# Kernel optimization log

Hardware: AMD Instinct MI355X
Metric: run time of the kernel (lower is better)

Reference implementation:

```python
import jax, jax.numpy as jnp
import numpy as np
from jax import lax

D_MODEL, D_INNER, N_STATE, DT_RANK, K = 1024, 2048, 16, 64, 3
B_SZ, SEQ = 2, 1024

def silu(v):
    return v * jax.nn.sigmoid(v)

def setup_inputs() -> dict:
    key = jax.random.key(0)
    ks = jax.random.split(key, 12)
    s = 0.02
    return {
        'x': jax.random.normal(ks[0], (B_SZ, SEQ, D_MODEL), jnp.float32),
        'A_log': jax.random.normal(ks[1], (D_INNER, N_STATE), jnp.float32) * 0.5,
        'W_in': jax.random.normal(ks[2], (D_MODEL, 2 * D_INNER), jnp.float32) * s,
        'b_in': jax.random.normal(ks[3], (2 * D_INNER,), jnp.float32) * s,
        'conv_w': jax.random.normal(ks[4], (D_INNER, 1, K), jnp.float32) * s,  # depthwise [O,I/g,K]
        'conv_b': jax.random.normal(ks[5], (D_INNER,), jnp.float32) * s,
        'W_x': jax.random.normal(ks[6], (D_INNER, DT_RANK + 2 * N_STATE), jnp.float32) * s,
        'W_dt': jax.random.normal(ks[7], (DT_RANK, D_INNER), jnp.float32) * s,
        'b_dt': jax.random.normal(ks[8], (D_INNER,), jnp.float32) * s,
        'W_out': jax.random.normal(ks[9], (D_INNER, D_MODEL), jnp.float32) * s,
        'b_out': jax.random.normal(ks[10], (D_MODEL,), jnp.float32) * s,
    }

def selective_scan(u, delta, A, B, C):
    # u, delta: [b,l,d]; A: [d,n]; B, C: [b,l,n]
    deltaA = jnp.exp(jnp.einsum('bld,dn->bldn', delta, A))          # [b,l,d,n]
    deltaBu = jnp.einsum('bld,bln,bld->bldn', delta, B, u)           # [b,l,d,n]
    h0 = jnp.zeros((u.shape[0], u.shape[2], A.shape[1]), u.dtype)    # [b,d,n]
    def step(h, inp):
        dA_t, dBu_t, C_t = inp
        h = dA_t * h + dBu_t
        y = jnp.einsum('bdn,bn->bd', h, C_t)
        return h, y
    xs = (jnp.moveaxis(deltaA, 1, 0), jnp.moveaxis(deltaBu, 1, 0), jnp.moveaxis(C, 1, 0))
    _, ys = lax.scan(step, h0, xs)                                   # [l,b,d]
    return jnp.moveaxis(ys, 0, 1)                                    # [b,l,d]

def reference(x, A_log, W_in, b_in, conv_w, conv_b, W_x, W_dt, b_dt, W_out, b_out):
    xr = x @ W_in + b_in                                             # [b,l,2*d_inner]
    u, res = jnp.split(xr, 2, axis=-1)
    # causal depthwise conv1d (pad left k-1, truncate == torch pad=k-1 then slice)
    uc = lax.conv_general_dilated(
        jnp.moveaxis(u, 1, 2), conv_w, window_strides=(1,),
        padding=[(K - 1, 0)], feature_group_count=D_INNER,
        dimension_numbers=('NCH', 'OIH', 'NCH'))
    u = silu(jnp.moveaxis(uc, 2, 1) + conv_b)                        # [b,l,d_inner]
    xp = u @ W_x                                                     # [b,l,dt_rank+2n]
    dt, Bm, Cm = jnp.split(xp, [DT_RANK, DT_RANK + N_STATE], axis=-1)
    delta = jax.nn.softplus(dt @ W_dt + b_dt)                        # [b,l,d_inner]
    A = -jnp.exp(A_log)                                              # [d_inner,n]
    y = selective_scan(u, delta, A, Bm, Cm)                          # [b,l,d_inner]
    y = y * silu(res)
    return y @ W_out + b_out
```

## Files before the change

### kernel.cpp

```cpp
#include <hip/hip_runtime.h>

#define D_MODEL 1024
#define D_INNER 2048
#define N_ST    16
#define DT_RANK 64
#define BSZ     2
#define SEQL    1024
#define NTOK    (BSZ*SEQL)
#define NC      64
#define LC      (SEQL/NC)

typedef __attribute__((ext_vector_type(4))) float f32x4;
typedef __attribute__((ext_vector_type(8))) short bf16x8;

__device__ __forceinline__ short f2b(float f) {
  unsigned u = __builtin_bit_cast(unsigned, f);
  u += 0x7fffu + ((u >> 16) & 1u);
  return (short)(u >> 16);
}

__device__ __forceinline__ float b2f(unsigned short s) {
  return __builtin_bit_cast(float, (unsigned)s << 16);
}

__device__ __forceinline__ void gload16(const void* g, void* l) {
  __builtin_amdgcn_global_load_lds(
      (const __attribute__((address_space(1))) void*)g,
      (__attribute__((address_space(3))) void*)l, 16, 0, 0);
}

template<int SOFTPLUS, int PARTIAL, int RESSPLIT, int OUTB16>
__global__ __launch_bounds__(256)
void gemm_kernel(const short* __restrict__ A, const short* __restrict__ Bm,
                 const float* __restrict__ bias, float* __restrict__ C,
                 short* __restrict__ upb, short* __restrict__ resb,
                 int M, int N, int K, int lda, int ldb, int ldc, int kChunk)
{
  __shared__ short sA[2][128 * 64];
  __shared__ short sB[2][128 * 64];
  const int tid  = threadIdx.x;
  const int lane = tid & 63;
  const int wave = tid >> 6;
  const int wr = wave >> 1, wc = wave & 1;
  const int lr = lane & 15, lg = lane >> 4;
  const int m0 = blockIdx.y * 128;
  const int n0 = blockIdx.x * 128;
  const int kStart = blockIdx.z * kChunk;
  int kEnd = kStart + kChunk; if (kEnd > K) kEnd = K;
  const int nt = (kEnd - kStart) >> 6;

  if (PARTIAL) C += (size_t)blockIdx.z * M * ldc;

  const int srow = lane >> 3;
  const int scol = ((lane & 7) ^ srow) * 8;
  const short* aS = A + (size_t)(m0 + wave * 32 + srow) * lda + scol + kStart;
  const short* bS = Bm + (size_t)(n0 + wave * 32 + srow) * ldb + scol + kStart;
  const int ldsOff = wave * 2048;

#define STAGE(buf, koff)                                                   \
  {                                                                        \
    _Pragma("unroll")                                                      \
    for (int i_ = 0; i_ < 4; ++i_) {                                       \
      gload16(aS + (size_t)(i_ * 8) * lda + (koff), &sA[buf][ldsOff + i_ * 512]); \
      gload16(bS + (size_t)(i_ * 8) * ldb + (koff), &sB[buf][ldsOff + i_ * 512]); \
    }                                                                      \
  }

  f32x4 acc[4][4];
#pragma unroll
  for (int i = 0; i < 4; ++i)
#pragma unroll
    for (int j = 0; j < 4; ++j) acc[i][j] = (f32x4){0.f, 0.f, 0.f, 0.f};

  STAGE(0, 0);

  for (int t = 0; t < nt; ++t) {
    const int cur = t & 1;
    if (t + 1 < nt) {
      STAGE(cur ^ 1, (t + 1) * 64);
      asm volatile("s_waitcnt vmcnt(8)" ::: "memory");
    } else {
      asm volatile("s_waitcnt vmcnt(0)" ::: "memory");
    }
    __builtin_amdgcn_s_barrier();

#pragma unroll
    for (int kk = 0; kk < 2; ++kk) {
      bf16x8 aF[4], bF[4];
#pragma unroll
      for (int mi = 0; mi < 4; ++mi) {
        const int row = wr * 64 + mi * 16 + lr;
        aF[mi] = *reinterpret_cast<const bf16x8*>(
            &sA[cur][row * 64 + (((kk * 4 + lg) ^ (lr & 7)) * 8)]);
      }
#pragma unroll
      for (int ni = 0; ni < 4; ++ni) {
        const int row = wc * 64 + ni * 16 + lr;
        bF[ni] = *reinterpret_cast<const bf16x8*>(
            &sB[cur][row * 64 + (((kk * 4 + lg) ^ (lr & 7)) * 8)]);
      }
#pragma unroll
      for (int mi = 0; mi < 4; ++mi)
#pragma unroll
        for (int ni = 0; ni < 4; ++ni)
          acc[mi][ni] = __builtin_amdgcn_mfma_f32_16x16x32_bf16(
              aF[mi], bF[ni], acc[mi][ni], 0, 0, 0);
    }
    __builtin_amdgcn_s_barrier();
  }
#undef STAGE

#pragma unroll
  for (int mi = 0; mi < 4; ++mi) {
    const int row = m0 + wr * 64 + mi * 16 + lg * 4;
#pragma unroll
    for (int ni = 0; ni < 4; ++ni) {
      const int col = n0 + wc * 64 + ni * 16 + lr;
      if (RESSPLIT) {
        const float bv = bias[col];
        if (col < 2048) {
#pragma unroll
          for (int j = 0; j < 4; ++j)
            upb[(size_t)(row + j) * 2048 + col] = f2b(acc[mi][ni][j] + bv);
        } else {
#pragma unroll
          for (int j = 0; j < 4; ++j) {
            float v = acc[mi][ni][j] + bv;
            resb[(size_t)(row + j) * 2048 + (col - 2048)] =
                f2b(v / (1.f + __expf(-v)));
          }
        }
      } else if (OUTB16) {
        const float bv = bias[col];
#pragma unroll
        for (int j = 0; j < 4; ++j) {
          float v = acc[mi][ni][j] + bv;
          if (SOFTPLUS) v = fmaxf(v, 0.f) + log1pf(__expf(-fabsf(v)));
          upb[(size_t)(row + j) * ldc + col] = f2b(v);
        }
      } else if (col < N) {
        float bv = (bias != nullptr && blockIdx.z == 0) ? bias[col] : 0.f;
#pragma unroll
        for (int j = 0; j < 4; ++j) {
          float v = acc[mi][ni][j] + bv;
          if (SOFTPLUS) v = fmaxf(v, 0.f) + log1pf(__expf(-fabsf(v)));
          C[(size_t)(row + j) * ldc + col] = v;
        }
      }
    }
  }
}

__device__ __forceinline__ void trans_body(const float* __restrict__ in,
                                           short* __restrict__ out,
                                           int R, int C, int bx, int by,
                                           short (*t)[33], int tidx)
{
  const int c0 = bx * 32, r0 = by * 32;
  const int cc = tidx & 31, rr = tidx >> 5;
#pragma unroll
  for (int i = 0; i < 4; ++i)
    t[rr + i * 8][cc] = f2b(in[(size_t)(r0 + rr + i * 8) * C + c0 + cc]);
  __syncthreads();
#pragma unroll
  for (int i = 0; i < 4; ++i)
    out[(size_t)(c0 + rr + i * 8) * R + r0 + cc] = t[cc][rr + i * 8];
}

#define PB_CAST  2048
#define PB_WIN   4096
#define PB_WX    192
#define PB_WDT   128
#define PB_WOUT  2048

__global__ __launch_bounds__(256)
void prep_kernel(const float* __restrict__ x,    const float* __restrict__ W_in,
                 const float* __restrict__ W_x,  const float* __restrict__ W_dt,
                 const float* __restrict__ W_out,
                 short* __restrict__ xb,  short* __restrict__ Wib,
                 short* __restrict__ Wxb, short* __restrict__ Wdtb,
                 short* __restrict__ Wob)
{
  __shared__ short t[32][33];
  const int bid = blockIdx.x, tidx = threadIdx.x;
  if (bid < PB_CAST) {
    const int i = bid * 256 + tidx;
    float4 v = *reinterpret_cast<const float4*>(x + (size_t)i * 4);
    *reinterpret_cast<short4*>(xb + (size_t)i * 4) =
        make_short4(f2b(v.x), f2b(v.y), f2b(v.z), f2b(v.w));
  } else if (bid < PB_CAST + PB_WIN) {
    const int b = bid - PB_CAST;
    trans_body(W_in, Wib, 1024, 4096, b % 128, b / 128, t, tidx);
  } else if (bid < PB_CAST + PB_WIN + PB_WX) {
    const int b = bid - PB_CAST - PB_WIN;
    trans_body(W_x, Wxb, 2048, 96, b % 3, b / 3, t, tidx);
  } else if (bid < PB_CAST + PB_WIN + PB_WX + PB_WDT) {
    const int b = bid - PB_CAST - PB_WIN - PB_WX;
    trans_body(W_dt, Wdtb, 64, 2048, b % 64, b / 64, t, tidx);
  } else {
    const int b = bid - PB_CAST - PB_WIN - PB_WX - PB_WDT;
    trans_body(W_out, Wob, 2048, 1024, b % 32, b / 32, t, tidx);
  }
}

__global__ __launch_bounds__(256)
void combine16_kernel(const float* __restrict__ part, float* __restrict__ xp,
                      short* __restrict__ dtb)
{
  const int gid = blockIdx.x * 256 + threadIdx.x;
  const int r = gid / 24, q = gid - r * 24;
  float4 s = make_float4(0.f, 0.f, 0.f, 0.f);
#pragma unroll
  for (int c = 0; c < 16; ++c) {
    const float4 v = *reinterpret_cast<const float4*>(
        part + (size_t)c * 2048 * 96 + (size_t)r * 96 + q * 4);
    s.x += v.x; s.y += v.y; s.z += v.z; s.w += v.w;
  }
  *reinterpret_cast<float4*>(xp + (size_t)r * 96 + q * 4) = s;
  if (q < 16)
    *reinterpret_cast<short4*>(dtb + (size_t)r * 64 + q * 4) =
        make_short4(f2b(s.x), f2b(s.y), f2b(s.z), f2b(s.w));
}

__global__ __launch_bounds__(256)
void combine4_kernel(const float* __restrict__ part, const float* __restrict__ bias,
                     float* __restrict__ out)
{
  const int gid = blockIdx.x * 256 + threadIdx.x;
  const int r = gid >> 8, c4 = gid & 255;
  const float4 bv = *reinterpret_cast<const float4*>(bias + c4 * 4);
  float4 s = bv;
#pragma unroll
  for (int z = 0; z < 4; ++z) {
    const float4 v = *reinterpret_cast<const float4*>(
        part + (size_t)z * 2048 * 1024 + (size_t)r * 1024 + c4 * 4);
    s.x += v.x; s.y += v.y; s.z += v.z; s.w += v.w;
  }
  *reinterpret_cast<float4*>(out + (size_t)r * 1024 + c4 * 4) = s;
}

__global__ __launch_bounds__(256)
void conv_silu_kernel(const unsigned short* __restrict__ up, const float* __restrict__ cw,
                      const float* __restrict__ cb, short* __restrict__ ub)
{
  int i  = blockIdx.x * 256 + threadIdx.x;
  int t  = i >> 9;
  int dq = (i & 511) << 2;
  int l  = t & (SEQL - 1);
  float4 w0 = *reinterpret_cast<const float4*>(cw + dq * 3);
  float4 w1 = *reinterpret_cast<const float4*>(cw + dq * 3 + 4);
  float4 w2 = *reinterpret_cast<const float4*>(cw + dq * 3 + 8);
  float4 bb = *reinterpret_cast<const float4*>(cb + dq);
  ushort4 X2 = *reinterpret_cast<const ushort4*>(up + (size_t)t * 2048 + dq);
  ushort4 z4; z4.x = z4.y = z4.z = z4.w = 0;
  ushort4 X1 = (l >= 1) ? *reinterpret_cast<const ushort4*>(up + (size_t)(t - 1) * 2048 + dq) : z4;
  ushort4 X0 = (l >= 2) ? *reinterpret_cast<const ushort4*>(up + (size_t)(t - 2) * 2048 + dq) : z4;
  float r0 = bb.x + w0.x * b2f(X0.x) + w0.y * b2f(X1.x) + w0.z * b2f(X2.x);
  float r1 = bb.y + w0.w * b2f(X0.y) + w1.x * b2f(X1.y) + w1.y * b2f(X2.y);
  float r2 = bb.z + w1.z * b2f(X0.z) + w1.w * b2f(X1.z) + w2.x * b2f(X2.z);
  float r3 = bb.w + w2.y * b2f(X0.w) + w2.z * b2f(X1.w) + w2.w * b2f(X2.w);
  float o0 = r0 / (1.f + __expf(-r0));
  float o1 = r1 / (1.f + __expf(-r1));
  float o2 = r2 / (1.f + __expf(-r2));
  float o3 = r3 / (1.f + __expf(-r3));
  *reinterpret_cast<short4*>(ub + (size_t)t * 2048 + dq) =
      make_short4(f2b(o0), f2b(o1), f2b(o2), f2b(o3));
}

__global__ __launch_bounds__(256, 4)
void scan_pass1(const unsigned short* __restrict__ deltab, const unsigned short* __restrict__ ub,
                const float* __restrict__ xp, const float* __restrict__ A_log,
                float* __restrict__ sdl, float* __restrict__ HS)
{
  const int d = blockIdx.y * 256 + threadIdx.x;
  const int c = blockIdx.x, b = blockIdx.z;
  const int t0 = (b << 10) + c * LC;
  float Ac[16];
#pragma unroll
  for (int q = 0; q < 4; ++q) {
    float4 a = *reinterpret_cast<const float4*>(A_log + (size_t)d * 16 + q * 4);
    Ac[q * 4 + 0] = -__expf(a.x); Ac[q * 4 + 1] = -__expf(a.y);
    Ac[q * 4 + 2] = -__expf(a.z); Ac[q * 4 + 3] = -__expf(a.w);
  }
  float h[16];
#pragma unroll
  for (int n = 0; n < 16; ++n) h[n] = 0.f;
  float sd = 0.f;
  const unsigned short* dp = deltab + (size_t)t0 * 2048 + d;
  const unsigned short* up = ub + (size_t)t0 * 2048 + d;
  const float* xb = xp + (size_t)t0 * 96 + DT_RANK;
#pragma unroll 4
  for (int t = 0; t < LC; ++t) {
    float dl = b2f(dp[(size_t)t * 2048]);
    float ul = b2f(up[(size_t)t * 2048]);
    float Bf[16];
#pragma unroll
    for (int q = 0; q < 4; ++q)
      *reinterpret_cast<float4*>(&Bf[q * 4]) =
          *reinterpret_cast<const float4*>(xb + (size_t)t * 96 + q * 4);
    float dlu = dl * ul;
    sd += dl;
#pragma unroll
    for (int n = 0; n < 16; ++n)
      h[n] = __expf(dl * Ac[n]) * h[n] + dlu * Bf[n];
  }
  sdl[((size_t)b * NC + c) * 2048 + d] = sd;
  float* hs = HS + (((size_t)b * NC + c) * 2048 + d) * 16;
#pragma unroll
  for (int q = 0; q < 4; ++q)
    *reinterpret_cast<float4*>(hs + q * 4) =
        make_float4(h[q * 4], h[q * 4 + 1], h[q * 4 + 2], h[q * 4 + 3]);
}

__global__ __launch_bounds__(256)
void scan_pass2(const float* __restrict__ sdl, const float* __restrict__ A_log,
                float* __restrict__ HS)
{
  const int gid = blockIdx.x * 256 + threadIdx.x;
  const int b = gid >> 15, rest = gid & 32767;
  const int d = rest >> 4;
  const float Ac = -__expf(A_log[rest]);
  float P[NC], S[NC];
#pragma unroll
  for (int c = 0; c < NC; ++c)
    P[c] = sdl[(((size_t)b * NC + c) << 11) + d];
#pragma unroll
  for (int c = 0; c < NC; ++c)
    S[c] = HS[(((size_t)b * NC + c) << 15) + rest];
#pragma unroll
  for (int c = 0; c < NC; ++c)
    P[c] = __expf(P[c] * Ac);
  float h = 0.f;
#pragma unroll
  for (int c = 0; c < NC; ++c) {
    HS[(((size_t)b * NC + c) << 15) + rest] = h;
    h = P[c] * h + S[c];
  }
}

__global__ __launch_bounds__(256, 4)
void scan_pass3(const unsigned short* __restrict__ deltab, const unsigned short* __restrict__ ub,
                const float* __restrict__ xp, const float* __restrict__ A_log,
                const float* __restrict__ HS, const unsigned short* __restrict__ rb,
                short* __restrict__ zb)
{
  const int d = blockIdx.y * 256 + threadIdx.x;
  const int c = blockIdx.x, b = blockIdx.z;
  const int t0 = (b << 10) + c * LC;
  float Ac[16];
#pragma unroll
  for (int q = 0; q < 4; ++q) {
    float4 a = *reinterpret_cast<const float4*>(A_log + (size_t)d * 16 + q * 4);
    Ac[q * 4 + 0] = -__expf(a.x); Ac[q * 4 + 1] = -__expf(a.y);
    Ac[q * 4 + 2] = -__expf(a.z); Ac[q * 4 + 3] = -__expf(a.w);
  }
  float h[16];
  const float* hs = HS + (((size_t)b * NC + c) * 2048 + d) * 16;
#pragma unroll
  for (int q = 0; q < 4; ++q) {
    float4 v = *reinterpret_cast<const float4*>(hs + q * 4);
    h[q * 4 + 0] = v.x; h[q * 4 + 1] = v.y; h[q * 4 + 2] = v.z; h[q * 4 + 3] = v.w;
  }
  const unsigned short* dp = deltab + (size_t)t0 * 2048 + d;
  const unsigned short* up = ub + (size_t)t0 * 2048 + d;
  const float* xb = xp + (size_t)t0 * 96 + DT_RANK;
  const float* xc = xp + (size_t)t0 * 96 + DT_RANK + N_ST;
  const unsigned short* rp = rb + (size_t)t0 * 2048 + d;
  short* zp = zb + (size_t)t0 * 2048 + d;
#pragma unroll 4
  for (int t = 0; t < LC; ++t) {
    float dl = b2f(dp[(size_t)t * 2048]);
    float ul = b2f(up[(size_t)t * 2048]);
    float rv = b2f(rp[(size_t)t * 2048]);
    float Bf[16], Cf[16];
#pragma unroll
    for (int q = 0; q < 4; ++q) {
      *reinterpret_cast<float4*>(&Bf[q * 4]) =
          *reinterpret_cast<const float4*>(xb + (size_t)t * 96 + q * 4);
      *reinterpret_cast<float4*>(&Cf[q * 4]) =
          *reinterpret_cast<const float4*>(xc + (size_t)t * 96 + q * 4);
    }
    float dlu = dl * ul;
    float p0 = 0.f, p1 = 0.f, p2 = 0.f, p3 = 0.f;
#pragma unroll
    for (int n = 0; n < 16; ++n) {
      h[n] = __expf(dl * Ac[n]) * h[n] + dlu * Bf[n];
      float t2 = h[n] * Cf[n];
      if ((n & 3) == 0) p0 += t2;
      else if ((n & 3) == 1) p1 += t2;
      else if ((n & 3) == 2) p2 += t2;
      else p3 += t2;
    }
    float p = (p0 + p1) + (p2 + p3);
    zp[(size_t)t * 2048] = f2b(p * rv);
  }
}

extern "C" void kernel_launch(void* const* d_in, const int* in_sizes, int n_in,
                              void* d_out, int out_size, void* d_ws, size_t ws_size,
                              hipStream_t stream)
{
  const float* x      = (const float*)d_in[0];
  const float* A_log  = (const float*)d_in[1];
  const float* W_in   = (const float*)d_in[2];
  const float* b_in   = (const float*)d_in[3];
  const float* conv_w = (const float*)d_in[4];
  const float* conv_b = (const float*)d_in[5];
  const float* W_x    = (const float*)d_in[6];
  const float* W_dt   = (const float*)d_in[7];
  const float* b_dt   = (const float*)d_in[8];
  const float* W_out  = (const float*)d_in[9];
  const float* b_out  = (const float*)d_in[10];
  float* out = (float*)d_out;

  char* p = (char*)d_ws;
  short* upb    = (short*)p; p += (size_t)NTOK * 2048 * 2;
  short* rb     = (short*)p; p += (size_t)NTOK * 2048 * 2;
  short* ub     = (short*)p; p += (size_t)NTOK * 2048 * 2;
  float* xp     = (float*)p; p += (size_t)NTOK * 96 * 4;
  short* dtb    = (short*)p; p += (size_t)NTOK * 64 * 2;
  short* deltab = (short*)p; p += (size_t)NTOK * 2048 * 2;
  short* zb     = (short*)p; p += (size_t)NTOK * 2048 * 2;
  short* xb     = (short*)p; p += (size_t)NTOK * 1024 * 2;
  short* Wib    = (short*)p; p += (size_t)4096 * 1024 * 2;
  short* Wxb    = (short*)p; p += (size_t)128 * 2048 * 2;
  short* Wdtb   = (short*)p; p += (size_t)2048 * 64 * 2;
  short* Wob    = (short*)p; p += (size_t)1024 * 2048 * 2;
  float* scr    = (float*)p; p += (size_t)4 * 2048 * 1024 * 4;
  float* xppart = scr;
  float* opart  = scr;
  float* sdl    = (float*)p; p += (size_t)BSZ * NC * 2048 * 4;
  float* HS     = (float*)p; p += (size_t)BSZ * NC * 2048 * 16 * 4;

  prep_kernel<<<dim3(PB_CAST + PB_WIN + PB_WX + PB_WDT + PB_WOUT), 256, 0, stream>>>(
      x, W_in, W_x, W_dt, W_out, xb, Wib, Wxb, Wdtb, Wob);

  gemm_kernel<0, 0, 1, 0><<<dim3(32, 16, 1), 256, 0, stream>>>(
      xb, Wib, b_in, nullptr, upb, rb, NTOK, 4096, 1024, 1024, 1024, 0, 1024);
  conv_silu_kernel<<<dim3(4096), 256, 0, stream>>>(
      (const unsigned short*)upb, conv_w, conv_b, ub);
  gemm_kernel<0, 1, 0, 0><<<dim3(1, 16, 16), 256, 0, stream>>>(
      ub, Wxb, nullptr, xppart, nullptr, nullptr, NTOK, 96, 2048, 2048, 2048, 96, 128);
  combine16_kernel<<<dim3(192), 256, 0, stream>>>(xppart, xp, dtb);
  gemm_kernel<1, 0, 0, 1><<<dim3(16, 16, 1), 256, 0, stream>>>(
      dtb, Wdtb, b_dt, nullptr, deltab, nullptr, NTOK, 2048, 64, 64, 64, 2048, 64);
  scan_pass1<<<dim3(NC, 8, BSZ), 256, 0, stream>>>(
      (const unsigned short*)deltab, (const unsigned short*)ub, xp, A_log, sdl, HS);
  scan_pass2<<<dim3(256), 256, 0, stream>>>(sdl, A_log, HS);
  scan_pass3<<<dim3(NC, 8, BSZ), 256, 0, stream>>>(
      (const unsigned short*)deltab, (const unsigned short*)ub, xp, A_log, HS,
      (const unsigned short*)rb, zb);
  gemm_kernel<0, 1, 0, 0><<<dim3(8, 16, 4), 256, 0, stream>>>(
      zb, Wob, nullptr, opart, nullptr, nullptr, NTOK, 1024, 2048, 2048, 2048, 1024, 512);
  combine4_kernel<<<dim3(2048), 256, 0, stream>>>(opart, b_out, out);
}
```

Baseline: 151.3 us.

## Fuse conv+SiLU into in-proj GEMM epilogue, bf16 out partials, fewer scan chunks

The in-projection GEMM now stages its bias-added u tile in LDS and computes the causal depthwise conv and SiLU in its epilogue. A small fixup kernel recomputes the two boundary rows of each 128-row tile. Block indices for that GEMM are remapped for locality. Output-projection split-K partials are stored as bf16 rather than fp32, and the scan chunk count drops from 64 to 32. Together these remove the standalone conv pass and halve partial-sum traffic, at the cost of extra rounding in the partial sums and less scan parallelism.

```diff
diff --git a/kernel.cpp b/kernel.cpp
--- a/kernel.cpp
+++ b/kernel.cpp
@@ -7,7 +7,7 @@
 #define BSZ     2
 #define SEQL    1024
 #define NTOK    (BSZ*SEQL)
-#define NC      64
+#define NC      32
 #define LC      (SEQL/NC)
 
 typedef __attribute__((ext_vector_type(4))) float f32x4;
@@ -34,6 +34,8 @@
 void gemm_kernel(const short* __restrict__ A, const short* __restrict__ Bm,
                  const float* __restrict__ bias, float* __restrict__ C,
                  short* __restrict__ upb, short* __restrict__ resb,
+                 const float* __restrict__ cw, const float* __restrict__ cb,
+                 short* __restrict__ ubuf,
                  int M, int N, int K, int lda, int ldb, int ldc, int kChunk)
 {
   __shared__ short sA[2][128 * 64];
@@ -43,13 +45,18 @@
   const int wave = tid >> 6;
   const int wr = wave >> 1, wc = wave & 1;
   const int lr = lane & 15, lg = lane >> 4;
-  const int m0 = blockIdx.y * 128;
-  const int n0 = blockIdx.x * 128;
+
+  int bx = blockIdx.x, by = blockIdx.y;
+  if (RESSPLIT) {
+    const int lin = by * 32 + bx;
+    const int lb = (lin & 7) * 64 + (lin >> 3);
+    bx = lb >> 4; by = lb & 15;
+  }
+  const int m0 = by * 128;
+  const int n0 = bx * 128;
   const int kStart = blockIdx.z * kChunk;
   int kEnd = kStart + kChunk; if (kEnd > K) kEnd = K;
   const int nt = (kEnd - kStart) >> 6;
-
-  if (PARTIAL) C += (size_t)blockIdx.z * M * ldc;
 
   const int srow = lane >> 3;
   const int scol = ((lane & 7) ^ srow) * 8;
@@ -110,19 +117,54 @@
   }
 #undef STAGE
 
-#pragma unroll
-  for (int mi = 0; mi < 4; ++mi) {
-    const int row = m0 + wr * 64 + mi * 16 + lg * 4;
-#pragma unroll
-    for (int ni = 0; ni < 4; ++ni) {
-      const int col = n0 + wc * 64 + ni * 16 + lr;
-      if (RESSPLIT) {
-        const float bv = bias[col];
-        if (col < 2048) {
-#pragma unroll
-          for (int j = 0; j < 4; ++j)
-            upb[(size_t)(row + j) * 2048 + col] = f2b(acc[mi][ni][j] + bv);
-        } else {
+  if (RESSPLIT) {
+    if (n0 < 2048) {
+      short (*sU)[128] = reinterpret_cast<short (*)[128]>(&sA[0][0]);
+#pragma unroll
+      for (int mi = 0; mi < 4; ++mi) {
+#pragma unroll
+        for (int ni = 0; ni < 4; ++ni) {
+          const int cl = wc * 64 + ni * 16 + lr;
+          const float bv = bias[n0 + cl];
+#pragma unroll
+          for (int j = 0; j < 4; ++j) {
+            const int rl = wr * 64 + mi * 16 + lg * 4 + j;
+            const short s = f2b(acc[mi][ni][j] + bv);
+            sU[rl][cl] = s;
+            if (rl < 2 || rl >= 126)
+              upb[(size_t)(m0 + rl) * 2048 + (n0 + cl)] = s;
+          }
+        }
+      }
+      __syncthreads();
+#pragma unroll
+      for (int ni = 0; ni < 4; ++ni) {
+        const int cl = wc * 64 + ni * 16 + lr;
+        const int col = n0 + cl;
+        const float w0 = cw[col * 3], w1 = cw[col * 3 + 1], w2 = cw[col * 3 + 2];
+        const float cbv = cb[col];
+#pragma unroll
+        for (int mi = 0; mi < 4; ++mi) {
+#pragma unroll
+          for (int j = 0; j < 4; ++j) {
+            const int rl = wr * 64 + mi * 16 + lg * 4 + j;
+            if (rl >= 2) {
+              float r = cbv + w0 * b2f((unsigned short)sU[rl - 2][cl])
+                            + w1 * b2f((unsigned short)sU[rl - 1][cl])
+                            + w2 * b2f((unsigned short)sU[rl][cl]);
+              ubuf[(size_t)(m0 + rl) * 2048 + col] = f2b(r / (1.f + __expf(-r)));
+            }
+          }
+        }
+      }
+    } else {
+#pragma unroll
+      for (int mi = 0; mi < 4; ++mi) {
+        const int row = m0 + wr * 64 + mi * 16 + lg * 4;
+#pragma unroll
+        for (int ni = 0; ni < 4; ++ni) {
+          const int col = n0 + wc * 64 + ni * 16 + lr;
+          const float bv = bias[col];
 #pragma unroll
           for (int j = 0; j < 4; ++j) {
             float v = acc[mi][ni][j] + bv;
@@ -130,7 +172,18 @@
                 f2b(v / (1.f + __expf(-v)));
           }
         }
-      } else if (OUTB16) {
+      }
+    }
+    return;
+  }
+
+#pragma unroll
+  for (int mi = 0; mi < 4; ++mi) {
+    const int row = m0 + wr * 64 + mi * 16 + lg * 4;
+#pragma unroll
+    for (int ni = 0; ni < 4; ++ni) {
+      const int col = n0 + wc * 64 + ni * 16 + lr;
+      if (OUTB16) {
         const float bv = bias[col];
 #pragma unroll
         for (int j = 0; j < 4; ++j) {
@@ -138,13 +191,19 @@
           if (SOFTPLUS) v = fmaxf(v, 0.f) + log1pf(__expf(-fabsf(v)));
           upb[(size_t)(row + j) * ldc + col] = f2b(v);
         }
+      } else if (PARTIAL == 2) {
+        short* Cs = (short*)C + (size_t)blockIdx.z * M * ldc;
+#pragma unroll
+        for (int j = 0; j < 4; ++j)
+          Cs[(size_t)(row + j) * ldc + col] = f2b(acc[mi][ni][j]);
       } else if (col < N) {
+        float* Cp = PARTIAL ? C + (size_t)blockIdx.z * M * ldc : C;
         float bv = (bias != nullptr && blockIdx.z == 0) ? bias[col] : 0.f;
 #pragma unroll
         for (int j = 0; j < 4; ++j) {
           float v = acc[mi][ni][j] + bv;
           if (SOFTPLUS) v = fmaxf(v, 0.f) + log1pf(__expf(-fabsf(v)));
-          C[(size_t)(row + j) * ldc + col] = v;
+          Cp[(size_t)(row + j) * ldc + col] = v;
         }
       }
     }
@@ -204,6 +263,33 @@
 }
 
 __global__ __launch_bounds__(256)
+void conv_fixup_kernel(const unsigned short* __restrict__ upb,
+                       const float* __restrict__ cw, const float* __restrict__ cb,
+                       short* __restrict__ ub)
+{
+  const int i  = blockIdx.x * 256 + threadIdx.x;
+  const int ti = i >> 9;
+  const int dq = (i & 511) << 2;
+  const int t  = (ti >> 1) * 128 + (ti & 1);
+  const int l  = t & (SEQL - 1);
+  float4 w0 = *reinterpret_cast<const float4*>(cw + dq * 3);
+  float4 w1 = *reinterpret_cast<const float4*>(cw + dq * 3 + 4);
+  float4 w2 = *reinterpret_cast<const float4*>(cw + dq * 3 + 8);
+  float4 bb = *reinterpret_cast<const float4*>(cb + dq);
+  ushort4 X2 = *reinterpret_cast<const ushort4*>(upb + (size_t)t * 2048 + dq);
+  ushort4 z4; z4.x = z4.y = z4.z = z4.w = 0;
+  ushort4 X1 = (l >= 1) ? *reinterpret_cast<const ushort4*>(upb + (size_t)(t - 1) * 2048 + dq) : z4;
+  ushort4 X0 = (l >= 2) ? *reinterpret_cast<const ushort4*>(upb + (size_t)(t - 2) * 2048 + dq) : z4;
+  float r0 = bb.x + w0.x * b2f(X0.x) + w0.y * b2f(X1.x) + w0.z * b2f(X2.x);
+  float r1 = bb.y + w0.w * b2f(X0.y) + w1.x * b2f(X1.y) + w1.y * b2f(X2.y);
+  float r2 = bb.z + w1.z * b2f(X0.z) + w1.w * b2f(X1.z) + w2.x * b2f(X2.z);
+  float r3 = bb.w + w2.y * b2f(X0.w) + w2.z * b2f(X1.w) + w2.w * b2f(X2.w);
+  *reinterpret_cast<short4*>(ub + (size_t)t * 2048 + dq) = make_short4(
+      f2b(r0 / (1.f + __expf(-r0))), f2b(r1 / (1.f + __expf(-r1))),
+      f2b(r2 / (1.f + __expf(-r2))), f2b(r3 / (1.f + __expf(-r3))));
+}
+
+__global__ __launch_bounds__(256)
 void combine16_kernel(const float* __restrict__ part, float* __restrict__ xp,
                       short* __restrict__ dtb)
 {
@@ -223,8 +309,8 @@
 }
 
 __global__ __launch_bounds__(256)
-void combine4_kernel(const float* __restrict__ part, const float* __restrict__ bias,
-                     float* __restrict__ out)
+void combine4_kernel(const unsigned short* __restrict__ part,
+                     const float* __restrict__ bias, float* __restrict__ out)
 {
   const int gid = blockIdx.x * 256 + threadIdx.x;
   const int r = gid >> 8, c4 = gid & 255;
@@ -232,39 +318,11 @@
   float4 s = bv;
 #pragma unroll
   for (int z = 0; z < 4; ++z) {
-    const float4 v = *reinterpret_cast<const float4*>(
+    const ushort4 v = *reinterpret_cast<const ushort4*>(
         part + (size_t)z * 2048 * 1024 + (size_t)r * 1024 + c4 * 4);
-    s.x += v.x; s.y += v.y; s.z += v.z; s.w += v.w;
+    s.x += b2f(v.x); s.y += b2f(v.y); s.z += b2f(v.z); s.w += b2f(v.w);
   }
   *reinterpret_cast<float4*>(out + (size_t)r * 1024 + c4 * 4) = s;
-}
-
-__global__ __launch_bounds__(256)
-void conv_silu_kernel(const unsigned short* __restrict__ up, const float* __restrict__ cw,
-                      const float* __restrict__ cb, short* __restrict__ ub)
-{
-  int i  = blockIdx.x * 256 + threadIdx.x;
-  int t  = i >> 9;
-  int dq = (i & 511) << 2;
-  int l  = t & (SEQL - 1);
-  float4 w0 = *reinterpret_cast<const float4*>(cw + dq * 3);
-  float4 w1 = *reinterpret_cast<const float4*>(cw + dq * 3 + 4);
-  float4 w2 = *reinterpret_cast<const float4*>(cw + dq * 3 + 8);
-  float4 bb = *reinterpret_cast<const float4*>(cb + dq);
-  ushort4 X2 = *reinterpret_cast<const ushort4*>(up + (size_t)t * 2048 + dq);
-  ushort4 z4; z4.x = z4.y = z4.z = z4.w = 0;
-  ushort4 X1 = (l >= 1) ? *reinterpret_cast<const ushort4*>(up + (size_t)(t - 1) * 2048 + dq) : z4;
-  ushort4 X0 = (l >= 2) ? *reinterpret_cast<const ushort4*>(up + (size_t)(t - 2) * 2048 + dq) : z4;
-  float r0 = bb.x + w0.x * b2f(X0.x) + w0.y * b2f(X1.x) + w0.z * b2f(X2.x);
-  float r1 = bb.y + w0.w * b2f(X0.y) + w1.x * b2f(X1.y) + w1.y * b2f(X2.y);
-  float r2 = bb.z + w1.z * b2f(X0.z) + w1.w * b2f(X1.z) + w2.x * b2f(X2.z);
-  float r3 = bb.w + w2.y * b2f(X0.w) + w2.z * b2f(X1.w) + w2.w * b2f(X2.w);
-  float o0 = r0 / (1.f + __expf(-r0));
-  float o1 = r1 / (1.f + __expf(-r1));
-  float o2 = r2 / (1.f + __expf(-r2));
-  float o3 = r3 / (1.f + __expf(-r3));
-  *reinterpret_cast<short4*>(ub + (size_t)t * 2048 + dq) =
-      make_short4(f2b(o0), f2b(o1), f2b(o2), f2b(o3));
 }
 
 __global__ __launch_bounds__(256, 4)
@@ -426,9 +484,9 @@
   short* Wxb    = (short*)p; p += (size_t)128 * 2048 * 2;
   short* Wdtb   = (short*)p; p += (size_t)2048 * 64 * 2;
   short* Wob    = (short*)p; p += (size_t)1024 * 2048 * 2;
-  float* scr    = (float*)p; p += (size_t)4 * 2048 * 1024 * 4;
-  float* xppart = scr;
-  float* opart  = scr;
+  char*  scr    = p;         p += (size_t)16 * 1024 * 1024;
+  float* xppart = (float*)scr;
+  short* opart  = (short*)scr;
   float* sdl    = (float*)p; p += (size_t)BSZ * NC * 2048 * 4;
   float* HS     = (float*)p; p += (size_t)BSZ * NC * 2048 * 16 * 4;
 
@@ -436,21 +494,26 @@
       x, W_in, W_x, W_dt, W_out, xb, Wib, Wxb, Wdtb, Wob);
 
   gemm_kernel<0, 0, 1, 0><<<dim3(32, 16, 1), 256, 0, stream>>>(
-      xb, Wib, b_in, nullptr, upb, rb, NTOK, 4096, 1024, 1024, 1024, 0, 1024);
-  conv_silu_kernel<<<dim3(4096), 256, 0, stream>>>(
+      xb, Wib, b_in, nullptr, upb, rb, conv_w, conv_b, ub,
+      NTOK, 4096, 1024, 1024, 1024, 0, 1024);
+  conv_fixup_kernel<<<dim3(128), 256, 0, stream>>>(
       (const unsigned short*)upb, conv_w, conv_b, ub);
   gemm_kernel<0, 1, 0, 0><<<dim3(1, 16, 16), 256, 0, stream>>>(
-      ub, Wxb, nullptr, xppart, nullptr, nullptr, NTOK, 96, 2048, 2048, 2048, 96, 128);
+      ub, Wxb, nullptr, xppart, nullptr, nullptr, nullptr, nullptr, nullptr,
+      NTOK, 96, 2048, 2048, 2048, 96, 128);
   combine16_kernel<<<dim3(192), 256, 0, stream>>>(xppart, xp, dtb);
   gemm_kernel<1, 0, 0, 1><<<dim3(16, 16, 1), 256, 0, stream>>>(
-      dtb, Wdtb, b_dt, nullptr, deltab, nullptr, NTOK, 2048, 64, 64, 64, 2048, 64);
+      dtb, Wdtb, b_dt, nullptr, deltab, nullptr, nullptr, nullptr, nullptr,
+      NTOK, 2048, 64, 64, 64, 2048, 64);
   scan_pass1<<<dim3(NC, 8, BSZ), 256, 0, stream>>>(
       (const unsigned short*)deltab, (const unsigned short*)ub, xp, A_log, sdl, HS);
   scan_pass2<<<dim3(256), 256, 0, stream>>>(sdl, A_log, HS);
   scan_pass3<<<dim3(NC, 8, BSZ), 256, 0, stream>>>(
       (const unsigned short*)deltab, (const unsigned short*)ub, xp, A_log, HS,
       (const unsigned short*)rb, zb);
-  gemm_kernel<0, 1, 0, 0><<<dim3(8, 16, 4), 256, 0, stream>>>(
-      zb, Wob, nullptr, opart, nullptr, nullptr, NTOK, 1024, 2048, 2048, 2048, 1024, 512);
-  combine4_kernel<<<dim3(2048), 256, 0, stream>>>(opart, b_out, out);
-}
+  gemm_kernel<0, 2, 0, 0><<<dim3(8, 16, 4), 256, 0, stream>>>(
+      zb, Wob, nullptr, (float*)opart, nullptr, nullptr, nullptr, nullptr, nullptr,
+      NTOK, 1024, 2048, 2048, 2048, 1024, 512);
+  combine4_kernel<<<dim3(2048), 256, 0, stream>>>(
+      (const unsigned short*)opart, b_out, out);
+}
```

Result: faster. 146.8 us (-3.0%).
